# Kernel optimization log

Hardware: AMD Instinct MI355X
Metric: run time of the kernel (lower is better)

The kernel has to match this reference:

```python
import jax, jax.numpy as jnp
import numpy as np

jax.config.update("jax_enable_x64", True)

N = 16          # particles per jet
B = 32          # number of jets
L2 = 1e-4       # qpth_l2_strength ('L2' form: Q = L2*I, p = flattened distance matrix)
ITERS = 20      # fixed interior-point iterations (converges well past solver tolerance)
SIGMA = 0.1     # centering parameter


def _build_G(n):
    # Inequality matrix, same layout as the torch code: G = [-I ; marginal-row-sums ; marginal-col-sums]
    m = n * n
    G1 = -np.eye(m)
    G2 = np.zeros((2 * n, m))
    for i in range(n):
        G2[i, i * n:(i + 1) * n] = 1.0      # sum_j x_{ij} <= w1_i
    for j in range(n):
        G2[n + j, j::n] = 1.0               # sum_i x_{ij} <= w2_j
    return jnp.asarray(np.concatenate([G1, G2], axis=0))  # [m + 2n, m]


def _solve_qp(p, h, b, G):
    """Batched infeasible-start primal-dual interior point solver for
    min 0.5*L2*||x||^2 + p.x  s.t.  G x <= h,  1.x = b  (same QP qpth solves)."""
    Bn, m = p.shape
    nin = G.shape[0]
    ones_m = jnp.ones((m,), p.dtype)
    x = jnp.zeros((Bn, m), p.dtype)
    s = jnp.ones((Bn, nin), p.dtype)
    z = jnp.ones((Bn, nin), p.dtype)
    y = jnp.zeros((Bn,), p.dtype)
    eye_m = jnp.eye(m, dtype=p.dtype)

    def step(carry, _):
        x, s, z, y = carry
        mu = jnp.mean(s * z, axis=1)                    # [B]
        rx = L2 * x + p + z @ G + y[:, None]            # dual residual   (A^T y = y * 1)
        rp = x @ G.T + s - h                            # primal ineq residual
        ra = x.sum(1) - b                               # primal eq residual
        rs = s * z - SIGMA * mu[:, None]                # complementarity residual
        d = z / s
        # H = Q + G^T diag(d) G  -> [B, m, m]
        H = L2 * eye_m + jnp.einsum('rk,br,rl->bkl', G, d, G)
        r1 = rx + ((z * rp - rs) / s) @ G
        Lc = jnp.linalg.cholesky(H)

        def chosolve(rhs):  # rhs [B, m] -> H^{-1} rhs
            t = jax.scipy.linalg.solve_triangular(Lc, rhs[..., None], lower=True)
            return jax.scipy.linalg.solve_triangular(Lc, t, lower=True, trans='T')[..., 0]

        u = chosolve(r1)
        v = chosolve(jnp.broadcast_to(ones_m, (Bn, m)))
        dy = (ra - u.sum(1)) / v.sum(1)                 # Schur complement on the 1-row equality
        dx = -u - v * dy[:, None]
        ds = -rp - dx @ G.T
        dz = (-rs - z * ds) / s
        # fraction-to-boundary step
        ds_safe = jnp.where(ds < 0, ds, -jnp.ones_like(ds))
        dz_safe = jnp.where(dz < 0, dz, -jnp.ones_like(dz))
        a_s = jnp.min(jnp.where(ds < 0, -s / ds_safe, jnp.inf), axis=1)
        a_z = jnp.min(jnp.where(dz < 0, -z / dz_safe, jnp.inf), axis=1)
        alpha = 0.99 * jnp.minimum(1.0, jnp.minimum(a_s, a_z))[:, None]
        x = x + alpha * dx
        s = s + alpha * ds
        z = z + alpha * dz
        y = y + alpha[:, 0] * dy
        return (x, s, z, y), None

    (x, s, z, y), _ = jax.lax.scan(step, (x, s, z, y), None, length=ITERS)
    return x


def setup_inputs() -> dict:
    key = jax.random.key(0)
    k1, k2 = jax.random.split(key)
    jets1 = jax.random.uniform(k1, (B, N, 3), dtype=jnp.float32)
    jets2 = jax.random.uniform(k2, (B, N, 3), dtype=jnp.float32)
    return {"jets1": jets1, "jets2": jets2}


def reference(jets1, jets2):
    j1 = jets1.astype(jnp.float64)
    j2 = jets2.astype(jnp.float64)
    nb, n = j1.shape[0], j1.shape[1]
    # pairwise (eta, phi) distances, same sign/epsilon as the torch code
    diffs = -(j1[:, :, None, :2] - j2[:, None, :, :2]) + 1e-12   # [B, n, n, 2]
    dists = jnp.sqrt(jnp.sum(diffs * diffs, axis=3))             # [B, n, n]
    w1 = j1[:, :, 2]
    w2 = j2[:, :, 2]
    p = dists.reshape(nb, n * n)
    h = jnp.concatenate([jnp.zeros((nb, n * n), p.dtype), w1, w2], axis=1)
    b = jnp.minimum(w1.sum(1), w2.sum(1))
    G = _build_G(n)
    flow = _solve_qp(p, h, b, G)                                  # [B, n*n]
    energy_diff = jnp.abs(w1.sum(1) - w2.sum(1))
    emds = jnp.sum(p * flow, axis=1) + energy_diff                # [B]
    return emds
```

## Files before the change

kernel.cpp:

```cpp
#include <hip/hip_runtime.h>
#include <math.h>

#define L2C  1e-4
#define SIGC 0.1
#define NITER 20

#if defined(__has_builtin)
#  if __has_builtin(__builtin_amdgcn_permlane16_swap) && __has_builtin(__builtin_amdgcn_permlane32_swap)
#    define HAVE_PLSWAP 1
#  endif
#  if __has_builtin(__builtin_amdgcn_rcp)
#    define HAVE_RCP64 1
#  endif
#  if __has_builtin(__builtin_amdgcn_mfma_f64_16x16x4f64)
#    define HAVE_MFMA64 1
#  endif
#endif
#ifndef HAVE_PLSWAP
#  define HAVE_PLSWAP 0
#endif
#ifndef HAVE_RCP64
#  define HAVE_RCP64 0
#endif
#ifndef HAVE_MFMA64
#  define HAVE_MFMA64 0
#endif

#if HAVE_MFMA64
typedef double v4d __attribute__((ext_vector_type(4)));
#endif

__device__ __forceinline__ double rld(double v, int lane) {
    union { double d; int i[2]; } u, r; u.d = v;
    r.i[0] = __builtin_amdgcn_readlane(u.i[0], lane);
    r.i[1] = __builtin_amdgcn_readlane(u.i[1], lane);
    return r.d;
}
template <int CTRL>
__device__ __forceinline__ double dppd(double v) {
    union { double d; int i[2]; } u, r; u.d = v;
    r.i[0] = __builtin_amdgcn_update_dpp(0, u.i[0], CTRL, 0xF, 0xF, true);
    r.i[1] = __builtin_amdgcn_update_dpp(0, u.i[1], CTRL, 0xF, 0xF, true);
    return r.d;
}
__device__ __forceinline__ double sum16d(double v) {
    v += dppd<0xB1>(v); v += dppd<0x4E>(v); v += dppd<0x124>(v); v += dppd<0x128>(v);
    return v;
}
template <int CTRL>
__device__ __forceinline__ float dppf(float v) {
    return __int_as_float(__builtin_amdgcn_update_dpp(0, __float_as_int(v), CTRL, 0xF, 0xF, true));
}
__device__ __forceinline__ float min16f(float v) {
    v = fminf(v, dppf<0xB1>(v)); v = fminf(v, dppf<0x4E>(v));
    v = fminf(v, dppf<0x124>(v)); v = fminf(v, dppf<0x128>(v));
    return v;
}
__device__ __forceinline__ float max16f(float v) {
    v = fmaxf(v, dppf<0xB1>(v)); v = fmaxf(v, dppf<0x4E>(v));
    v = fmaxf(v, dppf<0x124>(v)); v = fmaxf(v, dppf<0x128>(v));
    return v;
}
__device__ __forceinline__ double mkd(unsigned lo, unsigned hi) {
    union { unsigned u[2]; double d; } r; r.u[0] = lo; r.u[1] = hi; return r.d;
}
__device__ __forceinline__ void dsplit(double v, unsigned &lo, unsigned &hi) {
    union { double d; unsigned u[2]; } x; x.d = v; lo = x.u[0]; hi = x.u[1];
}
__device__ __forceinline__ double cross4d(double v) {
#if HAVE_PLSWAP
    unsigned lo, hi; dsplit(v, lo, hi);
    auto rl = __builtin_amdgcn_permlane16_swap(lo, lo, false, false);
    auto rh = __builtin_amdgcn_permlane16_swap(hi, hi, false, false);
    v = mkd(rl[0], rh[0]) + mkd(rl[1], rh[1]);
    dsplit(v, lo, hi);
    auto sl = __builtin_amdgcn_permlane32_swap(lo, lo, false, false);
    auto sh = __builtin_amdgcn_permlane32_swap(hi, hi, false, false);
    return mkd(sl[0], sh[0]) + mkd(sl[1], sh[1]);
#else
    v += __shfl_xor(v, 16, 64); v += __shfl_xor(v, 32, 64); return v;
#endif
}
__device__ __forceinline__ float cross4minf(float v) {
#if HAVE_PLSWAP
    auto a = __builtin_amdgcn_permlane16_swap(__float_as_uint(v), __float_as_uint(v), false, false);
    v = fminf(__uint_as_float(a[0]), __uint_as_float(a[1]));
    auto b = __builtin_amdgcn_permlane32_swap(__float_as_uint(v), __float_as_uint(v), false, false);
    return fminf(__uint_as_float(b[0]), __uint_as_float(b[1]));
#else
    v = fminf(v, __shfl_xor(v, 16, 64)); v = fminf(v, __shfl_xor(v, 32, 64)); return v;
#endif
}
__device__ __forceinline__ double drcp(double d) {
#if HAVE_RCP64
    double x = __builtin_amdgcn_rcp(d);
#else
    double x = (double)__builtin_amdgcn_rcpf((float)d);
#endif
    x = x * (2.0 - d * x);
    return x;
}
__device__ __forceinline__ float frcpf(float x) { return __builtin_amdgcn_rcpf(x); }

__global__ __launch_bounds__(64, 1) void emd_ip_kernel(const float* __restrict__ jets1,
                                                       const float* __restrict__ jets2,
                                                       float* __restrict__ out) {
    const int l = threadIdx.x;
    const int b = blockIdx.x;
    const int q = l & 15;
    const int r = l >> 4;

    __shared__ double invDl[16 * 17];
    __shared__ double Sst[16 * 17];
    __shared__ double Lst[16 * 17];
    __shared__ double Gst[2][16];
    __shared__ double Ast[16];
    __shared__ double Bst[16];

    const float* p1 = jets1 + b * 48;
    const float* p2 = jets2 + b * 48;

    double ax = (double)p1[3 * q], ay = (double)p1[3 * q + 1];
    double px[4];
#pragma unroll
    for (int c = 0; c < 4; c++) {
        int j = 4 * c + r;
        double d0 = ((double)p2[3 * j]     - ax) + 1e-12;
        double d1 = ((double)p2[3 * j + 1] - ay) + 1e-12;
        px[c] = sqrt(d0 * d0 + d1 * d1);
    }
    double h_rt = (double)p1[3 * q + 2];
    double h_ct[4];
#pragma unroll
    for (int c = 0; c < 4; c++) h_ct[c] = (double)p2[3 * (4 * c + r) + 2];

    double sw1 = sum16d(h_rt);
    double sw2 = sum16d((double)p2[3 * q + 2]);
    const double sB = fmin(sw1, sw2);
    const double sE = fabs(sw1 - sw2);

#if HAVE_PLSWAP
    auto pr16 = __builtin_amdgcn_permlane16_swap((unsigned)l, (unsigned)l, false, false);
    auto pr32 = __builtin_amdgcn_permlane32_swap((unsigned)l, (unsigned)l, false, false);
    const bool convOK = (__builtin_amdgcn_readfirstlane((int)pr16[0]) == 0) &&
                        (__builtin_amdgcn_readfirstlane((int)pr16[1]) == 16) &&
                        (__builtin_amdgcn_readfirstlane((int)pr32[0]) == 0) &&
                        (__builtin_amdgcn_readfirstlane((int)pr32[1]) == 32);
#else
    const bool convOK = false;
#endif

    bool mfmaOK = false;
#if HAVE_MFMA64
    {
        double Aval = 100.0 * q + r;
        double Bval = 1000.0 * r + q;
        v4d accT = {0.0, 0.0, 0.0, 0.0};
        accT = __builtin_amdgcn_mfma_f64_16x16x4f64(Aval, Bval, accT, 0, 0, 0);
        bool ok = true;
#pragma unroll
        for (int g = 0; g < 4; g++) {
            double di = 4.0 * r + g, dj = (double)q;
            double expect = 600000.0 * di + 400.0 * di * dj + 6.0 * dj + 14000.0;
            ok = ok && (accT[g] == expect);
        }
        mfmaOK = (__all(ok ? 1 : 0) != 0) && convOK;
    }
#endif

    double x[4] = {0, 0, 0, 0}, s[4] = {1, 1, 1, 1}, z[4] = {1, 1, 1, 1};
    double yv = 0.0;
    double s_rt = 1.0, z_rt = 1.0;
    double s_ct[4] = {1, 1, 1, 1}, z_ct[4] = {1, 1, 1, 1};
    double rsx = 0.0;
    double cs[4] = {0, 0, 0, 0};
    double ra = -sB;

    for (int it = 0; it < NITER; ++it) {
        double prt = s_rt * z_rt;
        double irt = drcp(prt);
        double is_rt = z_rt * irt, iz_rt = s_rt * irt;
        double srz = (s_rt * s_rt) * irt;
        double pct[4], is_ct[4], iz_ct[4];
#pragma unroll
        for (int c = 0; c < 4; c++) {
            pct[c] = s_ct[c] * z_ct[c];
            double ict = drcp(pct[c]);
            is_ct[c] = z_ct[c] * ict;
            iz_ct[c] = s_ct[c] * ict;
        }
        double szc[4], is_[4], iD[4];
#pragma unroll
        for (int c = 0; c < 4; c++) {
            szc[c] = s[c] * z[c];
            double tc = fma(L2C, s[c], z[c]);
            double ip = drcp(s[c] * tc);
            is_[c] = tc * ip;
            iD[c]  = (s[c] * s[c]) * ip;
            invDl[q * 17 + 4 * c + r] = iD[c];
        }

        double mub = szc[0] + szc[1] + szc[2] + szc[3]
                   + 0.25 * prt
                   + 0.0625 * (pct[0] + pct[1] + pct[2] + pct[3]);
        double mu = sum16d(cross4d(mub)) * (1.0 / 288.0);
        if (!(mu >= 1e-4)) break;
        double sgmu = SIGC * mu;

        double rp_rt = rsx + s_rt - h_rt;
        double rs_rt = prt - sgmu;
        double tt_rt = (z_rt * (rsx - h_rt) + sgmu) * is_rt;
        double rp_ct[4], rs_ct[4], tt_ct[4];
#pragma unroll
        for (int c = 0; c < 4; c++) {
            rp_ct[c] = cs[c] + s_ct[c] - h_ct[c];
            rs_ct[c] = pct[c] - sgmu;
            tt_ct[c] = (z_ct[c] * (cs[c] - h_ct[c]) + sgmu) * is_ct[c];
        }

        double rp[4], rs[4], r1[4], rD1[4];
#pragma unroll
        for (int c = 0; c < 4; c++) {
            double rx = L2C * x[c] + px[c] + (-z[c] + z_rt + z_ct[c]) + yv;
            rp[c] = s[c] - x[c];
            rs[c] = szc[c] - sgmu;
            double tk = (sgmu - z[c] * x[c]) * is_[c];
            r1[c] = rx - tk + tt_rt + tt_ct[c];
            rD1[c] = r1[c] * iD[c];
        }

        double rsI = cross4d(iD[0] + iD[1] + iD[2] + iD[3]);
        double rsR = cross4d(rD1[0] + rD1[1] + rD1[2] + rD1[3]);
        double csI[4];
#pragma unroll
        for (int c = 0; c < 4; c++) csI[c] = sum16d(iD[c]);

        double ar = drcp(srz + rsI);
        double aR = ar * rsR;
        double aI = ar * rsI;
        if (l < 16) Ast[l] = ar;

        double bb[4];
#pragma unroll
        for (int c = 0; c < 4; c++) {
            double gpR = sum16d(rD1[c] - aR * iD[c]);
            double gpI = csI[c] - sum16d(aI * iD[c]);
            bb[c] = s_ct[c] * iz_ct[c] + csI[c];
            if (q == 4 * c + r) { Gst[0][q] = gpR; Gst[1][q] = gpI; Bst[q] = bb[c]; }
        }

        double Sr[16];
#if HAVE_MFMA64
        if (mfmaOK) {
            double bbq = Bst[q];
            v4d acc;
#pragma unroll
            for (int g = 0; g < 4; g++) acc[g] = (4 * r + g == q) ? bbq : 0.0;
#pragma unroll
            for (int ch = 0; ch < 4; ch++) {
                int t = 4 * ch + r;
                double cellv = invDl[t * 17 + q];
                double af = -(Ast[t] * cellv);
                acc = __builtin_amdgcn_mfma_f64_16x16x4f64(af, cellv, acc, 0, 0, 0);
            }
#pragma unroll
            for (int g = 0; g < 4; g++) {
                unsigned lo, hi; dsplit(acc[g], lo, hi);
                auto s16l = __builtin_amdgcn_permlane16_swap(lo, lo, false, false);
                auto s16h = __builtin_amdgcn_permlane16_swap(hi, hi, false, false);
                auto aL = __builtin_amdgcn_permlane32_swap(s16l[0], s16l[0], false, false);
                auto aH = __builtin_amdgcn_permlane32_swap(s16h[0], s16h[0], false, false);
                auto bL = __builtin_amdgcn_permlane32_swap(s16l[1], s16l[1], false, false);
                auto bH = __builtin_amdgcn_permlane32_swap(s16h[1], s16h[1], false, false);
                Sr[0 * 4 + g] = mkd(aL[0], aH[0]);
                Sr[2 * 4 + g] = mkd(aL[1], aH[1]);
                Sr[1 * 4 + g] = mkd(bL[0], bH[0]);
                Sr[3 * 4 + g] = mkd(bL[1], bH[1]);
            }
        } else
#endif
        {
            double accA[4] = {0, 0, 0, 0}, accB[4] = {0, 0, 0, 0};
#pragma unroll
            for (int t = 0; t < 8; t++) {
                double wA = rld(ar, t) * invDl[t * 17 + q];
                double wB = rld(ar, t + 8) * invDl[(t + 8) * 17 + q];
#pragma unroll
                for (int c = 0; c < 4; c++) {
                    accA[c] += wA * invDl[t * 17 + 4 * c + r];
                    accB[c] += wB * invDl[(t + 8) * 17 + 4 * c + r];
                }
            }
#pragma unroll
            for (int c = 0; c < 4; c++)
                Sst[q * 17 + 4 * c + r] = ((q == 4 * c + r) ? bb[c] : 0.0) - (accA[c] + accB[c]);
#pragma unroll
            for (int j2 = 0; j2 < 16; j2++) Sr[j2] = Sst[q * 17 + j2];
        }

        double mrow = fabs(Sr[0]);
#pragma unroll
        for (int j2 = 1; j2 < 16; j2++) mrow = fmax(mrow, fabs(Sr[j2]));
        float mf = max16f((float)mrow);
        const double flo = fmax(1e-12 * (double)mf, 1e-280);

        double ysol = Gst[r >> 1][q];

        double invdv = 0.0;
        double pcand = 0.0;
#pragma unroll
        for (int kk = 0; kk < 16; kk++) {
            double praw = (kk == 0) ? rld(Sr[0], 0) : rld(pcand, kk);
            double dkk = fmax(praw, flo);
            double inv = drcp(dkk);
            invdv = (q == kk) ? inv : invdv;
            double Lc = Sr[kk] * inv;
            if (l < 16) Lst[kk * 17 + l] = Lc;
            if (kk < 15) pcand = Sr[kk + 1] - Sr[kk] * Lc;
            double t1 = rld(ysol, kk);
            double t2 = rld(ysol, kk + 32);
            double tt = (r < 2) ? t1 : t2;
            if (q > kk) ysol -= Lc * tt;
#pragma unroll
            for (int jj = kk + 1; jj < 16; jj++)
                Sr[jj] -= Sr[kk] * rld(Lc, jj);
            Sr[kk] = Lc;
        }

        ysol *= invdv;

        double LTr[16];
#pragma unroll
        for (int kk = 0; kk < 16; kk++) LTr[kk] = Lst[q * 17 + kk];

#pragma unroll
        for (int kk = 15; kk >= 0; kk--) {
            double t1 = rld(ysol, kk);
            double t2 = rld(ysol, kk + 32);
            double tt = (r < 2) ? t1 : t2;
            if (q < kk) ysol -= LTr[kk] * tt;
        }

        double qc1c[4], qcvc[4];
#pragma unroll
        for (int c = 0; c < 4; c++) {
            qc1c[c] = __shfl(ysol, 4 * c + r, 64);
            qcvc[c] = __shfl(ysol, 32 + 4 * c + r, 64);
        }

        double pr1 = iD[0]*qc1c[0] + iD[1]*qc1c[1] + iD[2]*qc1c[2] + iD[3]*qc1c[3];
        double prv = iD[0]*qcvc[0] + iD[1]*qcvc[1] + iD[2]*qcvc[2] + iD[3]*qcvc[3];
        double qr1 = ar * (rsR - cross4d(pr1));
        double qrv = ar * (rsI - cross4d(prv));

        double u[4], v[4];
#pragma unroll
        for (int c = 0; c < 4; c++) {
            u[c] = (r1[c] - qr1 - qc1c[c]) * iD[c];
            v[c] = (1.0  - qrv - qcvc[c]) * iD[c];
        }
        double urow = cross4d(u[0] + u[1] + u[2] + u[3]);
        double vrow = cross4d(v[0] + v[1] + v[2] + v[3]);
        double usum = sum16d(urow);
        double vsum = sum16d(vrow);
        double dy = (ra - usum) * drcp(vsum);

        double dx[4];
#pragma unroll
        for (int c = 0; c < 4; c++) dx[c] = -u[c] - v[c] * dy;
        double rsdx = -urow - vrow * dy;
        double csdx[4];
#pragma unroll
        for (int c = 0; c < 4; c++) csdx[c] = sum16d(dx[c]);
        double sumdx = -usum - vsum * dy;

        float amP = 1e30f, amD = 1e30f;
        double ds[4], dz[4];
#pragma unroll
        for (int c = 0; c < 4; c++) {
            ds[c] = dx[c] - rp[c];
            dz[c] = -(rs[c] + z[c] * ds[c]) * is_[c];
            if (ds[c] < 0.0) amP = fminf(amP, (float)s[c] * frcpf((float)(-ds[c])));
            if (dz[c] < 0.0) amD = fminf(amD, (float)z[c] * frcpf((float)(-dz[c])));
        }
        double ds_rt = -rp_rt - rsdx;
        double dz_rt = -(rs_rt + z_rt * ds_rt) * is_rt;
        if (ds_rt < 0.0) amP = fminf(amP, (float)s_rt * frcpf((float)(-ds_rt)));
        if (dz_rt < 0.0) amD = fminf(amD, (float)z_rt * frcpf((float)(-dz_rt)));
        double ds_ct[4], dz_ct[4];
#pragma unroll
        for (int c = 0; c < 4; c++) {
            ds_ct[c] = -rp_ct[c] - csdx[c];
            dz_ct[c] = -(rs_ct[c] + z_ct[c] * ds_ct[c]) * is_ct[c];
            if (ds_ct[c] < 0.0) amP = fminf(amP, (float)s_ct[c] * frcpf((float)(-ds_ct[c])));
            if (dz_ct[c] < 0.0) amD = fminf(amD, (float)z_ct[c] * frcpf((float)(-dz_ct[c])));
        }
        float aPf = min16f(cross4minf(amP));
        float aDf = min16f(cross4minf(amD));
        double alphaP = 0.99 * fmin(1.0, (double)aPf);
        double alphaD = 0.99 * fmin(1.0, (double)aDf);
        bool good = ((dy - dy) == 0.0);
        alphaP = good ? alphaP : 0.0;
        alphaD = good ? alphaD : 0.0;

#pragma unroll
        for (int c = 0; c < 4; c++) {
            x[c] += alphaP * dx[c];
            s[c] += alphaP * ds[c];
            z[c] += alphaD * dz[c];
            s_ct[c] += alphaP * ds_ct[c];
            z_ct[c] += alphaD * dz_ct[c];
            cs[c] += alphaP * csdx[c];
        }
        yv += alphaD * dy;
        s_rt += alphaP * ds_rt;
        z_rt += alphaD * dz_rt;
        rsx += alphaP * rsdx;
        ra  += alphaP * sumdx;
    }

    double e = sum16d(cross4d(px[0]*x[0] + px[1]*x[1] + px[2]*x[2] + px[3]*x[3]));
    if (l == 0) out[b] = (float)(e + sE);
}

extern "C" void kernel_launch(void* const* d_in, const int* in_sizes, int n_in,
                              void* d_out, int out_size, void* d_ws, size_t ws_size,
                              hipStream_t stream) {
    const float* jets1 = (const float*)d_in[0];
    const float* jets2 = (const float*)d_in[1];
    float* out = (float*)d_out;
    int B = in_sizes[0] / 48;
    emd_ip_kernel<<<dim3(B), dim3(64), 0, stream>>>(jets1, jets2, out);
}
```

Before: 112.1 us.

## Use 2x2 block LDL factorization for the 16x16 Schur complement solve

Replaces the scalar pivot-by-pivot Cholesky-like elimination of the 16x16 Schur matrix with a 2x2 block pivot scheme. The factorization and both triangular solves now handle two columns per step, which halves the serial dependency chain of cross-lane reads and reciprocals. The block diagonal inverse is applied at the end with a lane-pair shuffle. The regularization floor changes from a per-pivot clamp to a clamp on each 2x2 determinant, which may behave differently on ill-conditioned late iterations.

```diff
diff --git a/kernel.cpp b/kernel.cpp
--- a/kernel.cpp
+++ b/kernel.cpp
@@ -302,43 +302,51 @@
 #pragma unroll
         for (int j2 = 1; j2 < 16; j2++) mrow = fmax(mrow, fabs(Sr[j2]));
         float mf = max16f((float)mrow);
-        const double flo = fmax(1e-12 * (double)mf, 1e-280);
+        const double flo = 1e-12 * (double)mf;
+        const double flo2 = fmax(flo * flo, 1e-280);
 
         double ysol = Gst[r >> 1][q];
 
-        double invdv = 0.0;
-        double pcand = 0.0;
-#pragma unroll
-        for (int kk = 0; kk < 16; kk++) {
-            double praw = (kk == 0) ? rld(Sr[0], 0) : rld(pcand, kk);
-            double dkk = fmax(praw, flo);
-            double inv = drcp(dkk);
-            invdv = (q == kk) ? inv : invdv;
-            double Lc = Sr[kk] * inv;
-            if (l < 16) Lst[kk * 17 + l] = Lc;
-            if (kk < 15) pcand = Sr[kk + 1] - Sr[kk] * Lc;
-            double t1 = rld(ysol, kk);
-            double t2 = rld(ysol, kk + 32);
-            double tt = (r < 2) ? t1 : t2;
-            if (q > kk) ysol -= Lc * tt;
-#pragma unroll
-            for (int jj = kk + 1; jj < 16; jj++)
-                Sr[jj] -= Sr[kk] * rld(Lc, jj);
-            Sr[kk] = Lc;
-        }
-
-        ysol *= invdv;
+        double m0 = 0.0, m1 = 0.0;
+#pragma unroll
+        for (int p = 0; p < 8; p++) {
+            const int k0 = 2 * p, k1 = 2 * p + 1;
+            double W0 = Sr[k0], W1 = Sr[k1];
+            double av = rld(W0, k0);
+            double bv = rld(W0, k1);
+            double cv = rld(W1, k1);
+            double det = fmax(av * cv - bv * bv, flo2);
+            double idet = drcp(det);
+            double L0 = (W0 * cv - W1 * bv) * idet;
+            double L1 = (W1 * av - W0 * bv) * idet;
+            if (l < 16) { Lst[k0 * 17 + l] = L0; Lst[k1 * 17 + l] = L1; }
+            m0 = (q == k0) ? idet * cv : ((q == k1) ? idet * av : m0);
+            m1 = (q == k0 || q == k1) ? -(idet * bv) : m1;
+            double t0a = rld(ysol, k0), t0b = rld(ysol, k0 + 32);
+            double t1a = rld(ysol, k1), t1b = rld(ysol, k1 + 32);
+            double w0 = (r < 2) ? t0a : t0b;
+            double w1 = (r < 2) ? t1a : t1b;
+            if (q > k1) ysol -= L0 * w0 + L1 * w1;
+#pragma unroll
+            for (int jj = k1 + 1; jj < 16; jj++)
+                Sr[jj] -= L0 * rld(W0, jj) + L1 * rld(W1, jj);
+        }
+
+        double wpart = dppd<0xB1>(ysol);
+        ysol = m0 * ysol + m1 * wpart;
 
         double LTr[16];
 #pragma unroll
         for (int kk = 0; kk < 16; kk++) LTr[kk] = Lst[q * 17 + kk];
 
 #pragma unroll
-        for (int kk = 15; kk >= 0; kk--) {
-            double t1 = rld(ysol, kk);
-            double t2 = rld(ysol, kk + 32);
-            double tt = (r < 2) ? t1 : t2;
-            if (q < kk) ysol -= LTr[kk] * tt;
+        for (int p = 7; p >= 0; p--) {
+            const int k0 = 2 * p, k1 = 2 * p + 1;
+            double t0a = rld(ysol, k0), t0b = rld(ysol, k0 + 32);
+            double t1a = rld(ysol, k1), t1b = rld(ysol, k1 + 32);
+            double y0 = (r < 2) ? t0a : t0b;
+            double y1 = (r < 2) ? t1a : t1b;
+            if (q < k0) ysol -= LTr[k0] * y0 + LTr[k1] * y1;
         }
 
         double qc1c[4], qcvc[4];
```

Result: no change. 111.9 us (-0.2%).
